# Kernel tuning notes

Hardware: AMD Instinct MI355X
Metric: run time of the kernel (lower is better)

Reference implementation:

```python
import jax, jax.numpy as jnp
import numpy as np

BN_EPS = 1e-6


def setup_inputs() -> dict:
    key = jax.random.key(0)
    ks = jax.random.split(key, 6)
    B, N, K, D = 4, 40960, 16, 8
    coords = jax.random.normal(ks[0], (B, N, 3), dtype=jnp.float32)
    features = jax.random.normal(ks[1], (B, D, N, 1), dtype=jnp.float32)
    idx = jax.random.randint(ks[2], (B, N, K), 0, N, dtype=jnp.int32)
    dist = jax.random.uniform(ks[3], (B, N, K), dtype=jnp.float32)
    W = jax.random.normal(ks[4], (D, 10), dtype=jnp.float32) * 0.3
    b = jax.random.normal(ks[5], (D,), dtype=jnp.float32) * 0.1
    gamma = jnp.ones((D,), dtype=jnp.float32)
    beta = jnp.zeros((D,), dtype=jnp.float32)
    return {"coords": coords, "features": features, "idx": idx, "dist": dist,
            "W": W, "b": b, "gamma": gamma, "beta": beta}


def _locse(coords, features, idx, dist, W, b, gamma, beta):
    B, N, K = idx.shape
    D = W.shape[0]
    # gather neighbor coords: [B,N,K,3]
    neighbors = jax.vmap(lambda c, i: c[i])(coords, idx)
    center = jnp.broadcast_to(coords[:, :, None, :], (B, N, K, 3))
    # 10-channel relative-position encoding, channels-last [B,N,K,10]
    concat = jnp.concatenate(
        [center, neighbors, center - neighbors, dist[..., None]], axis=-1)
    # 1x1 conv (10 -> d), output [B,D,N,K]
    h = jnp.einsum('bnkc,dc->bdnk', concat, W) + b[None, :, None, None]
    # BatchNorm2d (training-mode batch stats over B,N,K per channel), eps=1e-6
    mean = jnp.mean(h, axis=(0, 2, 3), keepdims=True)
    var = jnp.var(h, axis=(0, 2, 3), keepdims=True)
    h = (h - mean) * jax.lax.rsqrt(var + BN_EPS)
    h = h * gamma[None, :, None, None] + beta[None, :, None, None]
    h = jax.nn.relu(h)
    # concat with broadcast input features -> [B, 2D, N, K]
    feats = jnp.broadcast_to(features, (B, D, N, K))
    return jnp.concatenate([h, feats], axis=1)


def reference(coords, features, idx, dist, W, b, gamma, beta):
    return _locse(coords, features, idx, dist, W, b, gamma, beta)
```

## Files before the change

### kernel.cpp

```cpp
#include <hip/hip_runtime.h>
#include <hip/hip_bf16.h>

constexpr int BB = 4;
constexpr int NN = 40960;
constexpr int KK = 16;
constexpr int DD = 8;
constexpr float BN_EPS = 1e-6f;

constexpr int STATS_BLOCKS = 512;
constexpr int STATS_THREADS = 256;


__global__ __launch_bounds__(STATS_THREADS) void locse_stats_kernel(
    const float* __restrict__ coords, const int* __restrict__ idx,
    const float* __restrict__ dist, const float* __restrict__ W,
    const float* __restrict__ bias, float* __restrict__ partials)
{
    __shared__ float sW[80];
    __shared__ float sb[8];
    if (threadIdx.x < 80) sW[threadIdx.x] = W[threadIdx.x];
    if (threadIdx.x < 8)  sb[threadIdx.x] = bias[threadIdx.x];
    __syncthreads();

    float sum[8] = {0.f, 0.f, 0.f, 0.f, 0.f, 0.f, 0.f, 0.f};
    float sq[8]  = {0.f, 0.f, 0.f, 0.f, 0.f, 0.f, 0.f, 0.f};

    const int total4 = BB * NN * (KK / 4);
    for (int t = blockIdx.x * blockDim.x + threadIdx.x; t < total4;
         t += gridDim.x * blockDim.x) {
        const int k4 = t & 3;
        const int bn = t >> 2;
        const int b  = bn / NN;
        const float* cc = coords + (size_t)bn * 3;
        const float cx = cc[0], cy = cc[1], cz = cc[2];

        const int base = (bn << 4) + (k4 << 2);
        const int4   j4 = *reinterpret_cast<const int4*>(idx + base);
        const float4 d4 = *reinterpret_cast<const float4*>(dist + base);
        const int   js[4] = {j4.x, j4.y, j4.z, j4.w};
        const float ds[4] = {d4.x, d4.y, d4.z, d4.w};

        #pragma unroll
        for (int kk = 0; kk < 4; ++kk) {
            const float* nc = coords + ((size_t)b * NN + js[kk]) * 3;
            const float nx = nc[0], ny = nc[1], nz = nc[2];
            const float c10[10] = {cx, cy, cz, nx, ny, nz,
                                   cx - nx, cy - ny, cz - nz, ds[kk]};
            #pragma unroll
            for (int d = 0; d < 8; ++d) {
                float h = sb[d];
                #pragma unroll
                for (int c = 0; c < 10; ++c) h = fmaf(sW[d * 10 + c], c10[c], h);
                sum[d] += h;
                sq[d]  += h * h;
            }
        }
    }

    #pragma unroll
    for (int v = 0; v < 8; ++v) {
        float s = sum[v], q = sq[v];
        #pragma unroll
        for (int off = 32; off > 0; off >>= 1) {
            s += __shfl_down(s, off, 64);
            q += __shfl_down(q, off, 64);
        }
        sum[v] = s; sq[v] = q;
    }

    __shared__ float wred[STATS_THREADS / 64][16];
    const int lane = threadIdx.x & 63;
    const int wid  = threadIdx.x >> 6;
    if (lane == 0) {
        #pragma unroll
        for (int v = 0; v < 8; ++v) {
            wred[wid][v]     = sum[v];
            wred[wid][8 + v] = sq[v];
        }
    }
    __syncthreads();
    if (threadIdx.x < 16) {
        float s = 0.f;
        #pragma unroll
        for (int w = 0; w < STATS_THREADS / 64; ++w) s += wred[w][threadIdx.x];
        partials[blockIdx.x * 16 + threadIdx.x] = s;
    }
}

__global__ __launch_bounds__(256) void locse_finalize_kernel(
    const float* __restrict__ partials, const float* __restrict__ W,
    const float* __restrict__ bias, const float* __restrict__ gamma,
    const float* __restrict__ beta, float* __restrict__ wp,
    float* __restrict__ bp)
{
    const int t = threadIdx.x;
    const int c = t & 15;
    float acc = 0.f;
    for (int i = t >> 4; i < STATS_BLOCKS; i += 16) acc += partials[i * 16 + c];

    __shared__ float red[256];
    __shared__ float tot[16];
    __shared__ float scale_s[8];
    red[t] = acc;
    __syncthreads();
    if (t < 16) {
        float s = 0.f;
        #pragma unroll
        for (int i = 0; i < 16; ++i) s += red[i * 16 + t];
        tot[t] = s;
    }
    __syncthreads();
    if (t < 8) {
        const float cnt  = (float)BB * (float)NN * (float)KK;
        const float mean = tot[t] / cnt;
        const float var  = tot[8 + t] / cnt - mean * mean;
        const float sc   = gamma[t] * rsqrtf(var + BN_EPS);
        scale_s[t] = sc;
        bp[t] = fmaf(bias[t] - mean, sc, beta[t]);
    }
    __syncthreads();
    if (t < 80) wp[t] = W[t] * scale_s[t / 10];
}

__global__ __launch_bounds__(256) void locse_out_kernel(
    const float* __restrict__ coords, const float* __restrict__ features,
    const int* __restrict__ idx, const float* __restrict__ dist,
    const float* __restrict__ wp, const float* __restrict__ bp,
    float* __restrict__ out)
{
    __shared__ float sW[80];
    __shared__ float sb[8];
    if (threadIdx.x < 80) sW[threadIdx.x] = wp[threadIdx.x];
    if (threadIdx.x < 8)  sb[threadIdx.x] = bp[threadIdx.x];
    __syncthreads();

    const int total4 = BB * NN * (KK / 4);
    for (int t = blockIdx.x * blockDim.x + threadIdx.x; t < total4;
         t += gridDim.x * blockDim.x) {
        const int k4 = t & 3;
        const int bn = t >> 2;
        const int n  = bn % NN;
        const int b  = bn / NN;
        const float* cc = coords + (size_t)bn * 3;
        const float cx = cc[0], cy = cc[1], cz = cc[2];

        const int base = (bn << 4) + (k4 << 2);
        const int4   j4 = *reinterpret_cast<const int4*>(idx + base);
        const float4 d4 = *reinterpret_cast<const float4*>(dist + base);
        const int   js[4] = {j4.x, j4.y, j4.z, j4.w};
        const float ds[4] = {d4.x, d4.y, d4.z, d4.w};

        float hv[8][4];
        #pragma unroll
        for (int kk = 0; kk < 4; ++kk) {
            const float* nc = coords + ((size_t)b * NN + js[kk]) * 3;
            const float nx = nc[0], ny = nc[1], nz = nc[2];
            const float c10[10] = {cx, cy, cz, nx, ny, nz,
                                   cx - nx, cy - ny, cz - nz, ds[kk]};
            #pragma unroll
            for (int d = 0; d < 8; ++d) {
                float h = sb[d];
                #pragma unroll
                for (int c = 0; c < 10; ++c) h = fmaf(sW[d * 10 + c], c10[c], h);
                hv[d][kk] = fmaxf(h, 0.f);
            }
        }

        const size_t outn = (size_t)b * 16 * NN * KK + (size_t)n * KK + (k4 << 2);
        #pragma unroll
        for (int d = 0; d < 8; ++d) {
            *reinterpret_cast<float4*>(out + outn + (size_t)d * NN * KK) =
                make_float4(hv[d][0], hv[d][1], hv[d][2], hv[d][3]);
        }
        #pragma unroll
        for (int d = 0; d < 8; ++d) {
            const float f = features[((size_t)b * DD + d) * NN + n];
            *reinterpret_cast<float4*>(out + outn + (size_t)(8 + d) * NN * KK) =
                make_float4(f, f, f, f);
        }
    }
}

extern "C" void kernel_launch(void* const* d_in, const int* in_sizes, int n_in,
                              void* d_out, int out_size, void* d_ws, size_t ws_size,
                              hipStream_t stream) {
    const float* coords   = (const float*)d_in[0];
    const float* features = (const float*)d_in[1];
    const int*   idx      = (const int*)d_in[2];
    const float* dist     = (const float*)d_in[3];
    const float* W        = (const float*)d_in[4];
    const float* bias     = (const float*)d_in[5];
    const float* gamma    = (const float*)d_in[6];
    const float* beta     = (const float*)d_in[7];
    float* out = (float*)d_out;

    float* wsf      = (float*)d_ws;
    float* partials = wsf;
    float* wp       = wsf + STATS_BLOCKS * 16;
    float* bp       = wp + 80;

    locse_stats_kernel<<<dim3(STATS_BLOCKS), dim3(STATS_THREADS), 0, stream>>>(
        coords, idx, dist, W, bias, partials);
    locse_finalize_kernel<<<dim3(1), dim3(256), 0, stream>>>(
        partials, W, bias, gamma, beta, wp, bp);

    const int total4 = BB * NN * (KK / 4);
    const int blocks = (total4 + 255) / 256;
    locse_out_kernel<<<dim3(blocks), dim3(256), 0, stream>>>(
        coords, features, idx, dist, wp, bp, out);
}
```

Before: 244.9 us.

## Fold conv weights algebraically, use nontemporal stores, enlarge stats blocks

Rewrites the 10-channel 1x1 conv by folding the center and relative-position weights into combined coefficients. The per-center part is computed once per thread, leaving four FMAs per neighbor per channel instead of ten. The output kernel drops its grid-stride loop in favor of one item per thread and writes through nontemporal stores to avoid cache pollution on the large output. The stats kernel moves to 1024-thread blocks. The output kernel is memory-bound, so the FMA savings may matter little, and nontemporal stores could affect write combining either way.

```diff
diff --git a/kernel.cpp b/kernel.cpp
--- a/kernel.cpp
+++ b/kernel.cpp
@@ -1,5 +1,4 @@
 #include <hip/hip_runtime.h>
-#include <hip/hip_bf16.h>
 
 constexpr int BB = 4;
 constexpr int NN = 40960;
@@ -7,26 +6,39 @@
 constexpr int DD = 8;
 constexpr float BN_EPS = 1e-6f;
 
-constexpr int STATS_BLOCKS = 512;
-constexpr int STATS_THREADS = 256;
-
-
-__global__ __launch_bounds__(STATS_THREADS) void locse_stats_kernel(
+constexpr int TOTAL4 = BB * NN * (KK / 4);
+
+constexpr int STATS_BLOCKS  = 512;
+constexpr int STATS_THREADS = 1024;
+
+typedef float f32x4 __attribute__((ext_vector_type(4)));
+
+
+
+__global__ __launch_bounds__(STATS_THREADS, 4) void locse_stats_kernel(
     const float* __restrict__ coords, const int* __restrict__ idx,
     const float* __restrict__ dist, const float* __restrict__ W,
     const float* __restrict__ bias, float* __restrict__ partials)
 {
-    __shared__ float sW[80];
-    __shared__ float sb[8];
-    if (threadIdx.x < 80) sW[threadIdx.x] = W[threadIdx.x];
-    if (threadIdx.x < 8)  sb[threadIdx.x] = bias[threadIdx.x];
+    __shared__ float sA[24];
+    __shared__ float sB[24];
+    __shared__ float sw9[8];
+    __shared__ float sbb[8];
+    if (threadIdx.x < 24) {
+        const int d = threadIdx.x / 3, j = threadIdx.x % 3;
+        sA[threadIdx.x] = W[d * 10 + j] + W[d * 10 + 6 + j];
+        sB[threadIdx.x] = W[d * 10 + 3 + j] - W[d * 10 + 6 + j];
+    }
+    if (threadIdx.x < 8) {
+        sw9[threadIdx.x] = W[threadIdx.x * 10 + 9];
+        sbb[threadIdx.x] = bias[threadIdx.x];
+    }
     __syncthreads();
 
     float sum[8] = {0.f, 0.f, 0.f, 0.f, 0.f, 0.f, 0.f, 0.f};
     float sq[8]  = {0.f, 0.f, 0.f, 0.f, 0.f, 0.f, 0.f, 0.f};
 
-    const int total4 = BB * NN * (KK / 4);
-    for (int t = blockIdx.x * blockDim.x + threadIdx.x; t < total4;
+    for (int t = blockIdx.x * blockDim.x + threadIdx.x; t < TOTAL4;
          t += gridDim.x * blockDim.x) {
         const int k4 = t & 3;
         const int bn = t >> 2;
@@ -34,6 +46,13 @@
         const float* cc = coords + (size_t)bn * 3;
         const float cx = cc[0], cy = cc[1], cz = cc[2];
 
+        float cA[8];
+        #pragma unroll
+        for (int d = 0; d < 8; ++d)
+            cA[d] = fmaf(sA[d * 3 + 2], cz,
+                    fmaf(sA[d * 3 + 1], cy,
+                    fmaf(sA[d * 3 + 0], cx, sbb[d])));
+
         const int base = (bn << 4) + (k4 << 2);
         const int4   j4 = *reinterpret_cast<const int4*>(idx + base);
         const float4 d4 = *reinterpret_cast<const float4*>(dist + base);
@@ -44,13 +63,12 @@
         for (int kk = 0; kk < 4; ++kk) {
             const float* nc = coords + ((size_t)b * NN + js[kk]) * 3;
             const float nx = nc[0], ny = nc[1], nz = nc[2];
-            const float c10[10] = {cx, cy, cz, nx, ny, nz,
-                                   cx - nx, cy - ny, cz - nz, ds[kk]};
             #pragma unroll
             for (int d = 0; d < 8; ++d) {
-                float h = sb[d];
-                #pragma unroll
-                for (int c = 0; c < 10; ++c) h = fmaf(sW[d * 10 + c], c10[c], h);
+                float h = fmaf(sw9[d], ds[kk],
+                          fmaf(sB[d * 3 + 2], nz,
+                          fmaf(sB[d * 3 + 1], ny,
+                          fmaf(sB[d * 3 + 0], nx, cA[d]))));
                 sum[d] += h;
                 sq[d]  += h * h;
             }
@@ -128,56 +146,70 @@
     const float* __restrict__ wp, const float* __restrict__ bp,
     float* __restrict__ out)
 {
-    __shared__ float sW[80];
-    __shared__ float sb[8];
-    if (threadIdx.x < 80) sW[threadIdx.x] = wp[threadIdx.x];
-    if (threadIdx.x < 8)  sb[threadIdx.x] = bp[threadIdx.x];
-    __syncthreads();
-
-    const int total4 = BB * NN * (KK / 4);
-    for (int t = blockIdx.x * blockDim.x + threadIdx.x; t < total4;
-         t += gridDim.x * blockDim.x) {
-        const int k4 = t & 3;
-        const int bn = t >> 2;
-        const int n  = bn % NN;
-        const int b  = bn / NN;
-        const float* cc = coords + (size_t)bn * 3;
-        const float cx = cc[0], cy = cc[1], cz = cc[2];
-
-        const int base = (bn << 4) + (k4 << 2);
-        const int4   j4 = *reinterpret_cast<const int4*>(idx + base);
-        const float4 d4 = *reinterpret_cast<const float4*>(dist + base);
-        const int   js[4] = {j4.x, j4.y, j4.z, j4.w};
-        const float ds[4] = {d4.x, d4.y, d4.z, d4.w};
-
-        float hv[8][4];
-        #pragma unroll
-        for (int kk = 0; kk < 4; ++kk) {
-            const float* nc = coords + ((size_t)b * NN + js[kk]) * 3;
-            const float nx = nc[0], ny = nc[1], nz = nc[2];
-            const float c10[10] = {cx, cy, cz, nx, ny, nz,
-                                   cx - nx, cy - ny, cz - nz, ds[kk]};
-            #pragma unroll
-            for (int d = 0; d < 8; ++d) {
-                float h = sb[d];
-                #pragma unroll
-                for (int c = 0; c < 10; ++c) h = fmaf(sW[d * 10 + c], c10[c], h);
-                hv[d][kk] = fmaxf(h, 0.f);
-            }
-        }
-
-        const size_t outn = (size_t)b * 16 * NN * KK + (size_t)n * KK + (k4 << 2);
+    __shared__ float sA[24];
+    __shared__ float sB[24];
+    __shared__ float sw9[8];
+    __shared__ float sbb[8];
+    if (threadIdx.x < 24) {
+        const int d = threadIdx.x / 3, j = threadIdx.x % 3;
+        sA[threadIdx.x] = wp[d * 10 + j] + wp[d * 10 + 6 + j];
+        sB[threadIdx.x] = wp[d * 10 + 3 + j] - wp[d * 10 + 6 + j];
+    }
+    if (threadIdx.x < 8) {
+        sw9[threadIdx.x] = wp[threadIdx.x * 10 + 9];
+        sbb[threadIdx.x] = bp[threadIdx.x];
+    }
+    __syncthreads();
+
+    const int t = blockIdx.x * blockDim.x + threadIdx.x;
+    const int k4 = t & 3;
+    const int bn = t >> 2;
+    const int b  = bn / NN;
+    const int n  = bn - b * NN;
+    const float* cc = coords + (size_t)bn * 3;
+    const float cx = cc[0], cy = cc[1], cz = cc[2];
+
+    float cA[8];
+    #pragma unroll
+    for (int d = 0; d < 8; ++d)
+        cA[d] = fmaf(sA[d * 3 + 2], cz,
+                fmaf(sA[d * 3 + 1], cy,
+                fmaf(sA[d * 3 + 0], cx, sbb[d])));
+
+    const int base = (bn << 4) + (k4 << 2);
+    const int4   j4 = *reinterpret_cast<const int4*>(idx + base);
+    const float4 d4 = *reinterpret_cast<const float4*>(dist + base);
+    const int   js[4] = {j4.x, j4.y, j4.z, j4.w};
+    const float ds[4] = {d4.x, d4.y, d4.z, d4.w};
+
+    float hv[8][4];
+    #pragma unroll
+    for (int kk = 0; kk < 4; ++kk) {
+        const float* nc = coords + ((size_t)b * NN + js[kk]) * 3;
+        const float nx = nc[0], ny = nc[1], nz = nc[2];
         #pragma unroll
         for (int d = 0; d < 8; ++d) {
-            *reinterpret_cast<float4*>(out + outn + (size_t)d * NN * KK) =
-                make_float4(hv[d][0], hv[d][1], hv[d][2], hv[d][3]);
-        }
-        #pragma unroll
-        for (int d = 0; d < 8; ++d) {
-            const float f = features[((size_t)b * DD + d) * NN + n];
-            *reinterpret_cast<float4*>(out + outn + (size_t)(8 + d) * NN * KK) =
-                make_float4(f, f, f, f);
-        }
+            const float h = fmaf(sw9[d], ds[kk],
+                            fmaf(sB[d * 3 + 2], nz,
+                            fmaf(sB[d * 3 + 1], ny,
+                            fmaf(sB[d * 3 + 0], nx, cA[d]))));
+            hv[d][kk] = fmaxf(h, 0.f);
+        }
+    }
+
+    const size_t outn = (size_t)b * 16 * NN * KK + (size_t)n * KK + (k4 << 2);
+    #pragma unroll
+    for (int d = 0; d < 8; ++d) {
+        f32x4* p = reinterpret_cast<f32x4*>(out + outn + (size_t)d * NN * KK);
+        const f32x4 v = {hv[d][0], hv[d][1], hv[d][2], hv[d][3]};
+        __builtin_nontemporal_store(v, p);
+    }
+    #pragma unroll
+    for (int d = 0; d < 8; ++d) {
+        const float f = features[((size_t)b * DD + d) * NN + n];
+        f32x4* p = reinterpret_cast<f32x4*>(out + outn + (size_t)(8 + d) * NN * KK);
+        const f32x4 v = {f, f, f, f};
+        __builtin_nontemporal_store(v, p);
     }
 }
 
@@ -204,8 +236,7 @@
     locse_finalize_kernel<<<dim3(1), dim3(256), 0, stream>>>(
         partials, W, bias, gamma, beta, wp, bp);
 
-    const int total4 = BB * NN * (KK / 4);
-    const int blocks = (total4 + 255) / 256;
+    const int blocks = TOTAL4 / 256;
     locse_out_kernel<<<dim3(blocks), dim3(256), 0, stream>>>(
         coords, features, idx, dist, wp, bp, out);
 }
```

After: 269.7 us. 10.1% more time.
